# Optimization experiments

Hardware: AMD Instinct MI355X
Metric: run time of the kernel (lower is better)

## Reference

```python
import jax, jax.numpy as jnp
import numpy as np

N = 50000   # nodes per node type
D = 256     # in_dim == out_dim
H = 8       # num heads
DK = D // H # 32
E = 500000  # edges per edge type
LN_EPS = 1e-5


def setup_inputs() -> dict:
    key = jax.random.key(0)
    ks = jax.random.split(key, 16)
    w = lambda k, shape: jax.random.normal(k, shape, dtype=jnp.float32) * 0.05
    xav = np.sqrt(6.0 / (DK + DK))
    return {
        'feats': jax.random.normal(ks[0], (2, N, D), dtype=jnp.float32),
        'Wk': w(ks[1], (2, D, D)), 'bk': jnp.zeros((2, D), jnp.float32),
        'Wq': w(ks[2], (2, D, D)), 'bq': jnp.zeros((2, D), jnp.float32),
        'Wv': w(ks[3], (2, D, D)), 'bv': jnp.zeros((2, D), jnp.float32),
        'Wa': w(ks[4], (2, D, D)), 'ba': jnp.zeros((2, D), jnp.float32),
        'ln_w': jnp.ones((2, D), jnp.float32), 'ln_b': jnp.zeros((2, D), jnp.float32),
        'skip': jnp.ones((2,), jnp.float32),
        'mu': jnp.ones((2, H), jnp.float32),
        'w_att': jax.random.uniform(ks[5], (2, H, DK, DK), jnp.float32, -xav, xav),
        'w_msg': jax.random.uniform(ks[6], (2, H, DK, DK), jnp.float32, -xav, xav),
        'src': jax.random.randint(ks[7], (2, E), 0, N, dtype=jnp.int32),
        'dst': jax.random.randint(ks[8], (2, E), 0, N, dtype=jnp.int32),
    }


def _edge_softmax(scores, seg, n):
    # scores: (E, H); softmax over edges sharing the same destination node
    m = jax.ops.segment_max(scores, seg, num_segments=n)          # (N, H)
    e = jnp.exp(scores - m[seg])
    s = jax.ops.segment_sum(e, seg, num_segments=n)               # (N, H)
    return e / s[seg]


def _forward(feats, Wk, bk, Wq, bq, Wv, bv, Wa, ba, ln_w, ln_b, skip,
             mu, w_att, w_msg, src, dst):
    # canonical etypes: 0 = author->paper, 1 = paper->author
    stypes, dtypes = (0, 1), (1, 0)
    scale = 1.0 / jnp.sqrt(jnp.asarray(DK, feats.dtype))
    h = [None, None]
    for et in range(2):
        st, dt = stypes[et], dtypes[et]
        s_idx, d_idx = src[et], dst[et]
        k = (feats[st] @ Wk[st] + bk[st]).reshape(N, H, DK)
        k = jnp.einsum('nhi,hij->nhj', k, w_att[et])
        v = (feats[st] @ Wv[st] + bv[st]).reshape(N, H, DK)
        v = jnp.einsum('nhi,hij->nhj', v, w_msg[et])
        q = (feats[dt] @ Wq[dt] + bq[dt]).reshape(N, H, DK)
        t = jnp.einsum('ehd,ehd->eh', q[d_idx], k[s_idx])         # (E, H)
        attn = _edge_softmax(t * mu[et] * scale, d_idx, N)        # (E, H)
        msg = v[s_idx] * attn[..., None]                          # (E, H, DK)
        h[dt] = jax.ops.segment_sum(msg, d_idx, num_segments=N).reshape(N, D)
    h = jnp.stack(h)  # (2, N, D); each ntype receives from exactly one etype

    trans = jnp.einsum('tnd,tde->tne', h, Wa) + ba[:, None, :]
    alpha = jax.nn.sigmoid(skip)[:, None, None]
    out = alpha * trans + (1.0 - alpha) * feats
    mean = out.mean(-1, keepdims=True)
    var = out.var(-1, keepdims=True)
    out = (out - mean) * jax.lax.rsqrt(var + LN_EPS)
    return out * ln_w[:, None, :] + ln_b[:, None, :]


def reference(feats, Wk, bk, Wq, bq, Wv, bv, Wa, ba, ln_w, ln_b, skip,
              mu, w_att, w_msg, src, dst):
    return _forward(feats, Wk, bk, Wq, bq, Wv, bv, Wa, ba, ln_w, ln_b, skip,
                    mu, w_att, w_msg, src, dst)
```

## Files before the change

### kernel.cpp

```cpp
#include <hip/hip_runtime.h>
#include <hip/hip_bf16.h>

#define D 256
#define H 8
#define DK 32

typedef unsigned short ushort_t;
typedef unsigned int uint_t;
typedef __attribute__((ext_vector_type(4))) float floatx4;
typedef __attribute__((ext_vector_type(2))) float floatx2;
typedef __attribute__((ext_vector_type(8))) short shortx8;
typedef __attribute__((ext_vector_type(8))) unsigned short ushortx8;

typedef __attribute__((address_space(3))) void lds_void_t;
typedef const __attribute__((address_space(1))) void gbl_void_t;

__device__ __forceinline__ float b2f(ushort_t u) {
    return __uint_as_float(((uint_t)u) << 16);
}
__device__ __forceinline__ floatx2 b2x2(uint_t u) {
    floatx2 r;
    r.x = __uint_as_float(u << 16);
    r.y = __uint_as_float(u & 0xffff0000u);
    return r;
}
__device__ __forceinline__ ushort_t f2b(float f) {
    uint_t u = __float_as_uint(f);
    uint_t r = (u + 0x7FFFu + ((u >> 16) & 1u)) >> 16;
    return (ushort_t)r;
}
__device__ __forceinline__ void async_cp16(const void* g, void* l) {
    __builtin_amdgcn_global_load_lds((gbl_void_t*)g, (lds_void_t*)l, 16, 0, 0);
}

__global__ void cvt_bf16(const float* __restrict__ in, ushort_t* __restrict__ out, size_t n4) {
    size_t i = (size_t)blockIdx.x * blockDim.x + threadIdx.x;
    if (i >= n4) return;
    float4 v = ((const float4*)in)[i];
    ushort4 o;
    o.x = f2b(v.x); o.y = f2b(v.y); o.z = f2b(v.z); o.w = f2b(v.w);
    ((ushort4*)out)[i] = o;
}

__global__ void zero_int(int* __restrict__ p, int n) {
    int i = blockIdx.x * blockDim.x + threadIdx.x;
    if (i < n) p[i] = 0;
}

__global__ void fold_weights(const float* __restrict__ Wk, const float* __restrict__ bk,
                             const float* __restrict__ Wv, const float* __restrict__ bv,
                             const float* __restrict__ w_att, const float* __restrict__ w_msg,
                             float* __restrict__ Wkc, float* __restrict__ bkc,
                             float* __restrict__ Wvc, float* __restrict__ bvc) {
    int r = blockIdx.x, et = blockIdx.y, which = blockIdx.z;
    int tid = threadIdx.x;
    const float* Wsrc = (which ? Wv : Wk) + (size_t)et * D * D + (size_t)r * D;
    const float* wt   = (which ? w_msg : w_att) + (size_t)et * H * DK * DK;
    float* Wdst = (which ? Wvc : Wkc) + (size_t)et * D * D;
    __shared__ float wrow[D];
    wrow[tid] = Wsrc[tid];
    __syncthreads();
    int h = tid >> 5, j = tid & 31;
    const float* wth = wt + h * DK * DK;
    float acc = 0.f;
#pragma unroll 8
    for (int i = 0; i < DK; i++) acc += wrow[h * 32 + i] * wth[i * 32 + j];
    Wdst[(size_t)r * D + tid] = acc;
    if (r == 0) {
        const float* bsrc = (which ? bv : bk) + et * D;
        float* bdst = (which ? bvc : bkc) + et * D;
        float bacc = 0.f;
#pragma unroll 8
        for (int i = 0; i < DK; i++) bacc += bsrc[h * 32 + i] * wth[i * 32 + j];
        bdst[tid] = bacc;
    }
}

__global__ void pack_weights(const float* __restrict__ Wq, const float* __restrict__ bq,
                             const float* __restrict__ Wkc, const float* __restrict__ bkc,
                             const float* __restrict__ Wvc, const float* __restrict__ bvc,
                             const float* __restrict__ Wa,
                             ushort_t* __restrict__ WT_all, ushort_t* __restrict__ WaT,
                             float* __restrict__ bias_all) {
    int idx = blockIdx.x * blockDim.x + threadIdx.x;
    const int NW = 2 * 768 * 256;
    if (idx < NW) {
        int t = idx / (768 * 256);
        int rem = idx - t * 768 * 256;
        int n = rem >> 8, k = rem & 255;
        int sec = n >> 8, nn = n & 255;
        const float* W = (sec == 0) ? Wq : (sec == 1) ? Wkc : Wvc;
        WT_all[idx] = f2b(W[(size_t)t * D * D + (size_t)k * D + nn]);
    } else if (idx < NW + 2 * 256 * 256) {
        int r = idx - NW;
        int t = r / (256 * 256);
        int rem = r - t * 256 * 256;
        int n = rem >> 8, k = rem & 255;
        WaT[r] = f2b(Wa[(size_t)t * D * D + (size_t)k * D + n]);
    }
    if (idx < 2 * 768) {
        int t = idx / 768, n = idx % 768;
        int sec = n >> 8, nn = n & 255;
        const float* b = (sec == 0) ? bq : (sec == 1) ? bkc : bvc;
        bias_all[idx] = b[t * D + nn];
    }
}

#define TM 128
#define TN 128
#define TKK 64
__launch_bounds__(256)
__global__ void gemm_mfma(const ushort_t* __restrict__ A0, int lda, size_t aStr,
                          const ushort_t* __restrict__ BT0, size_t bStr,
                          const float* __restrict__ bias0, int biasStr,
                          ushort_t* __restrict__ C0, int ldc, size_t cStr, int M) {
    __shared__ ushort_t As[TM * TKK];
    __shared__ ushort_t Bs[TN * TKK];
    int tid = threadIdx.x;
    int w = tid >> 6, lane = tid & 63;
    int t = blockIdx.z;
    const ushort_t* A  = A0 + (size_t)t * aStr;
    const ushort_t* BT = BT0 + (size_t)t * bStr;
    const float* bias  = bias0 + (size_t)t * biasStr;
    ushort_t* C        = C0 + (size_t)t * cStr;

    int nwg  = gridDim.x * gridDim.y;
    int orig = blockIdx.y * gridDim.x + blockIdx.x;
    int q = nwg >> 3, r = nwg & 7;
    int xcd = orig & 7, loc = orig >> 3;
    int wgid = (xcd < r ? xcd * (q + 1) : r * (q + 1) + (xcd - r) * q) + loc;
    int ncol = gridDim.y;
    int rowt = wgid / ncol;
    int colt = wgid - rowt * ncol;
    int bm = rowt * TM;
    int bn = colt * TN;

    int wm = (w & 1) * 64, wn = (w >> 1) * 64;

    floatx4 acc[4][4] = {};

    int sr8    = lane >> 3;
    int swzcol = 8 * ((lane & 7) ^ sr8);

    int fr = lane & 15, fq = lane >> 4;
    int fswz = (fr & 7) * 8;

    for (int kc = 0; kc < 256; kc += TKK) {
#pragma unroll
        for (int j = 0; j < 4; j++) {
            int rr = w * 32 + j * 8;
            int gr = bm + rr + sr8; if (gr >= M) gr = M - 1;
            async_cp16(A + (size_t)gr * lda + kc + swzcol, As + rr * TKK);
            int gn = bn + rr + sr8;
            async_cp16(BT + (size_t)gn * 256 + kc + swzcol, Bs + rr * TKK);
        }
        __builtin_amdgcn_s_waitcnt(0x0F70);
        __syncthreads();

#pragma unroll
        for (int kk = 0; kk < 2; kk++) {
            shortx8 af[4], bf[4];
            int rcol = (kk * 32) ^ fswz;
#pragma unroll
            for (int i = 0; i < 4; i++)
                af[i] = *(const shortx8*)(As + (wm + i * 16 + fr) * TKK + ((kk * 32 + fq * 8) ^ fswz));
#pragma unroll
            for (int j = 0; j < 4; j++)
                bf[j] = *(const shortx8*)(Bs + (wn + j * 16 + fr) * TKK + ((kk * 32 + fq * 8) ^ fswz));
#pragma unroll
            for (int i = 0; i < 4; i++)
#pragma unroll
                for (int j = 0; j < 4; j++)
                    acc[i][j] = __builtin_amdgcn_mfma_f32_16x16x32_bf16(af[i], bf[j], acc[i][j], 0, 0, 0);
            (void)rcol;
        }
        __syncthreads();
    }

#pragma unroll
    for (int i = 0; i < 4; i++) {
#pragma unroll
        for (int j = 0; j < 4; j++) {
            int col = bn + wn + j * 16 + fr;
            float bv = bias[col];
#pragma unroll
            for (int rr = 0; rr < 4; rr++) {
                int row = bm + wm + i * 16 + fq * 4 + rr;
                if (row < M) C[(size_t)row * ldc + col] = f2b(acc[i][j][rr] + bv);
            }
        }
    }
}

__global__ void count_deg(const int* __restrict__ dst, int* __restrict__ deg,
                          int N, int E) {
    int i = blockIdx.x * blockDim.x + threadIdx.x;
    if (i >= 2 * E) return;
    int et = i / E, e = i - et * E;
    int d = dst[(size_t)et * E + e];
    atomicAdd(&deg[(1 - et) * N + d], 1);
}

__launch_bounds__(256)
__global__ void scan_blocks(int* __restrict__ deg, int* __restrict__ bsum, int n) {
    __shared__ int wsum[4];
    int tid = threadIdx.x, lane = tid & 63, w = tid >> 6;
    int i = blockIdx.x * 256 + tid;
    int v = (i < n) ? deg[i] : 0;
    int x = v;
#pragma unroll
    for (int off = 1; off < 64; off <<= 1) {
        int y = __shfl_up(x, off);
        if (lane >= off) x += y;
    }
    if (lane == 63) wsum[w] = x;
    __syncthreads();
    int add = 0;
    if (w > 0) add += wsum[0];
    if (w > 1) add += wsum[1];
    if (w > 2) add += wsum[2];
    int incl = x + add;
    if (i < n) deg[i] = incl - v;
    if (tid == 255) bsum[blockIdx.x] = incl;
}

__launch_bounds__(512)
__global__ void scan_tops(int* __restrict__ bsum, int* __restrict__ row_ptr,
                          int nb, int n) {
    __shared__ int wsum[8];
    int tid = threadIdx.x, lane = tid & 63, w = tid >> 6;
    int v = (tid < nb) ? bsum[tid] : 0;
    int x = v;
#pragma unroll
    for (int off = 1; off < 64; off <<= 1) {
        int y = __shfl_up(x, off);
        if (lane >= off) x += y;
    }
    if (lane == 63) wsum[w] = x;
    __syncthreads();
    int add = 0;
    for (int j = 0; j < w; j++) add += wsum[j];
    int incl = x + add;
    if (tid < nb) bsum[tid] = incl - v;
    if (tid == nb - 1) row_ptr[n] = incl;
}

__launch_bounds__(256)
__global__ void scan_apply(const int* __restrict__ excl, const int* __restrict__ bsum,
                           int* __restrict__ row_ptr, int* __restrict__ cursor, int n) {
    int i = blockIdx.x * 256 + threadIdx.x;
    if (i >= n) return;
    int e = excl[i] + bsum[blockIdx.x];
    row_ptr[i] = e;
    cursor[i] = e;
}

__global__ void fill_edges(const int* __restrict__ src, const int* __restrict__ dst,
                           int* __restrict__ cursor, int* __restrict__ ebuf,
                           int N, int E) {
    int i = blockIdx.x * blockDim.x + threadIdx.x;
    if (i >= 2 * E) return;
    int et = i / E, e = i - et * E;
    int d = dst[(size_t)et * E + e];
    int s = src[(size_t)et * E + e];
    int pos = atomicAdd(&cursor[(1 - et) * N + d], 1);
    ebuf[pos] = s;
}

__launch_bounds__(256)
__global__ void node_aggregate(ushort_t* __restrict__ QKV, const float* __restrict__ mu,
                               const int* __restrict__ row_ptr, const int* __restrict__ ebuf,
                               int N) {
    int wid = (blockIdx.x * blockDim.x + threadIdx.x) >> 6;
    int lane = threadIdx.x & 63;
    if (wid >= 2 * N) return;
    int dt = (wid >= N) ? 1 : 0;
    int et = 1 - dt;
    int l = lane & 31;
    int half = lane >> 5;
    int h = l >> 2;

    uint4 qu = ((const uint4*)(QKV + (size_t)wid * 768))[l];
    floatx2 q01 = b2x2(qu.x), q23 = b2x2(qu.y), q45 = b2x2(qu.z), q67 = b2x2(qu.w);
    float sc = mu[et * H + h] * 0.17677669529663687f;
    int beg = row_ptr[wid], end = row_ptr[wid + 1];
    const ushort_t* KVb = QKV + (size_t)et * N * 768 + l * 8;

    floatx2 a01 = {0.f, 0.f}, a23 = {0.f, 0.f}, a45 = {0.f, 0.f}, a67 = {0.f, 0.f};
    float ssum = 0.f;

#define AGG_COMPUTE(kk, vv)                                              \
    {                                                                    \
        floatx2 pv = q01 * b2x2(kk.x);                                   \
        pv += q23 * b2x2(kk.y);                                          \
        pv += q45 * b2x2(kk.z);                                          \
        pv += q67 * b2x2(kk.w);                                          \
        float pp = pv.x + pv.y;                                          \
        pp += __shfl_xor(pp, 1);                                         \
        pp += __shfl_xor(pp, 2);                                         \
        float ex = __expf(pp * sc);                                      \
        ssum += ex;                                                      \
        floatx2 e2 = {ex, ex};                                           \
        a01 += e2 * b2x2(vv.x);                                          \
        a23 += e2 * b2x2(vv.y);                                          \
        a45 += e2 * b2x2(vv.z);                                          \
        a67 += e2 * b2x2(vv.w);                                          \
    }

    int p = beg + half;
    uint4 kA = {}, vA = {}, kB = {}, vB = {};
    int sC = 0, sD = 0;
    if (p < end) {
        int sA = ebuf[p];
        const ushort_t* r0 = KVb + (size_t)sA * 768;
        kA = *(const uint4*)(r0 + 256);
        vA = *(const uint4*)(r0 + 512);
        sC = (p + 4 < end) ? ebuf[p + 4] : sA;
    }
    if (p + 2 < end) {
        int sB = ebuf[p + 2];
        const ushort_t* r1 = KVb + (size_t)sB * 768;
        kB = *(const uint4*)(r1 + 256);
        vB = *(const uint4*)(r1 + 512);
        sD = (p + 6 < end) ? ebuf[p + 6] : sB;
    }
    while (p < end) {
        uint4 nk = kA, nv = vA;
        int sE = sC;
        if (p + 4 < end) {
            const ushort_t* rr = KVb + (size_t)sC * 768;
            nk = *(const uint4*)(rr + 256);
            nv = *(const uint4*)(rr + 512);
            if (p + 8 < end) sE = ebuf[p + 8];
        }
        AGG_COMPUTE(kA, vA);
        kA = nk; vA = nv; sC = sE;
        p += 2;
        if (p >= end) break;
        nk = kB; nv = vB; sE = sD;
        if (p + 4 < end) {
            const ushort_t* rr = KVb + (size_t)sD * 768;
            nk = *(const uint4*)(rr + 256);
            nv = *(const uint4*)(rr + 512);
            if (p + 8 < end) sE = ebuf[p + 8];
        }
        AGG_COMPUTE(kB, vB);
        kB = nk; vB = nv; sD = sE;
        p += 2;
    }
#undef AGG_COMPUTE

    ssum += __shfl_xor(ssum, 32);
    a01.x += __shfl_xor(a01.x, 32); a01.y += __shfl_xor(a01.y, 32);
    a23.x += __shfl_xor(a23.x, 32); a23.y += __shfl_xor(a23.y, 32);
    a45.x += __shfl_xor(a45.x, 32); a45.y += __shfl_xor(a45.y, 32);
    a67.x += __shfl_xor(a67.x, 32); a67.y += __shfl_xor(a67.y, 32);
    float r = (ssum > 0.f) ? 1.0f / ssum : 0.0f;
    if (half == 0) {
        ushortx8 hv;
        hv[0] = f2b(a01.x * r); hv[1] = f2b(a01.y * r);
        hv[2] = f2b(a23.x * r); hv[3] = f2b(a23.y * r);
        hv[4] = f2b(a45.x * r); hv[5] = f2b(a45.y * r);
        hv[6] = f2b(a67.x * r); hv[7] = f2b(a67.y * r);
        ((ushortx8*)(QKV + (size_t)wid * 768))[l] = hv;
    }
}

__launch_bounds__(256)
__global__ void skip_ln(const ushort_t* __restrict__ trans, const float* __restrict__ feats,
                        const float* __restrict__ lnw, const float* __restrict__ lnb,
                        const float* __restrict__ skip, float* __restrict__ out, int N) {
    int wid = (blockIdx.x * blockDim.x + threadIdx.x) >> 6;
    int lane = threadIdx.x & 63;
    if (wid >= 2 * N) return;
    int t = (wid >= N) ? 1 : 0;
    float alpha = 1.0f / (1.0f + __expf(-skip[t]));
    float beta = 1.0f - alpha;
    size_t base = (size_t)wid * D;
    ushort4 tu = ((const ushort4*)(trans + base))[lane];
    float4 fu = ((const float4*)(feats + base))[lane];
    float x0 = alpha * b2f(tu.x) + beta * fu.x;
    float x1 = alpha * b2f(tu.y) + beta * fu.y;
    float x2 = alpha * b2f(tu.z) + beta * fu.z;
    float x3 = alpha * b2f(tu.w) + beta * fu.w;
    float s  = x0 + x1 + x2 + x3;
    float sq = x0 * x0 + x1 * x1 + x2 * x2 + x3 * x3;
#pragma unroll
    for (int off = 1; off < 64; off <<= 1) {
        s  += __shfl_xor(s,  off);
        sq += __shfl_xor(sq, off);
    }
    float mean = s * (1.0f / 256.0f);
    float var  = sq * (1.0f / 256.0f) - mean * mean;
    float r = rsqrtf(var + 1e-5f);
    float4 w4 = ((const float4*)(lnw + t * D))[lane];
    float4 b4 = ((const float4*)(lnb + t * D))[lane];
    float4 o;
    o.x = (x0 - mean) * r * w4.x + b4.x;
    o.y = (x1 - mean) * r * w4.y + b4.y;
    o.z = (x2 - mean) * r * w4.z + b4.z;
    o.w = (x3 - mean) * r * w4.w + b4.w;
    ((float4*)(out + base))[lane] = o;
}

extern "C" void kernel_launch(void* const* d_in, const int* in_sizes, int n_in,
                              void* d_out, int out_size, void* d_ws, size_t ws_size,
                              hipStream_t stream) {
    const float* feats = (const float*)d_in[0];
    const float* Wk    = (const float*)d_in[1];
    const float* bk    = (const float*)d_in[2];
    const float* Wq    = (const float*)d_in[3];
    const float* bq    = (const float*)d_in[4];
    const float* Wv    = (const float*)d_in[5];
    const float* bv    = (const float*)d_in[6];
    const float* Wa    = (const float*)d_in[7];
    const float* ba    = (const float*)d_in[8];
    const float* ln_w  = (const float*)d_in[9];
    const float* ln_b  = (const float*)d_in[10];
    const float* skip  = (const float*)d_in[11];
    const float* mu    = (const float*)d_in[12];
    const float* w_att = (const float*)d_in[13];
    const float* w_msg = (const float*)d_in[14];
    const int*   src   = (const int*)d_in[15];
    const int*   dst   = (const int*)d_in[16];
    float* out = (float*)d_out;

    const int N = in_sizes[0] / (2 * D);
    const int E = in_sizes[15] / 2;
    const int NN = 2 * N;
    const size_t ND2 = 2 * (size_t)N * D;

    float* ws = (float*)d_ws;
    size_t off = 0;
    float* Wkc  = ws + off; off += 2 * (size_t)D * D;
    float* Wvc  = ws + off; off += 2 * (size_t)D * D;
    float* bkc  = ws + off; off += 2 * D;
    float* bvc  = ws + off; off += 2 * D;
    float* bias_all = ws + off; off += 2 * 768;
    ushort_t* WT_all = (ushort_t*)(ws + off); off += 2 * 768 * 256 / 2;
    ushort_t* WaT    = (ushort_t*)(ws + off); off += 2 * 256 * 256 / 2;
    ushort_t* featsb = (ushort_t*)(ws + off); off += ND2 / 2;
    ushort_t* QKV    = (ushort_t*)(ws + off); off += 2 * (size_t)N * 768 / 2;
    int* deg     = (int*)(ws + off); off += NN;
    int* row_ptr = (int*)(ws + off); off += NN + 1;
    int* cursor  = (int*)(ws + off); off += NN + 1;
    int* ebuf    = (int*)(ws + off); off += 2 * (size_t)E;
    int* bsum    = (int*)(ws + off); off += 512;

    const int nb = (NN + 255) / 256;

    zero_int<<<(NN + 255) / 256, 256, 0, stream>>>(deg, NN);
    count_deg<<<(2 * E + 255) / 256, 256, 0, stream>>>(dst, deg, N, E);
    scan_blocks<<<nb, 256, 0, stream>>>(deg, bsum, NN);
    scan_tops<<<1, 512, 0, stream>>>(bsum, row_ptr, nb, NN);
    scan_apply<<<nb, 256, 0, stream>>>(deg, bsum, row_ptr, cursor, NN);
    fill_edges<<<(2 * E + 255) / 256, 256, 0, stream>>>(src, dst, cursor, ebuf, N, E);

    fold_weights<<<dim3(D, 2, 2), 256, 0, stream>>>(Wk, bk, Wv, bv, w_att, w_msg,
                                                    Wkc, bkc, Wvc, bvc);
    pack_weights<<<(2 * 768 * 256 + 2 * 256 * 256 + 255) / 256, 256, 0, stream>>>(
        Wq, bq, Wkc, bkc, Wvc, bvc, Wa, WT_all, WaT, bias_all);

    cvt_bf16<<<(unsigned)((ND2 / 4 + 255) / 256), 256, 0, stream>>>(feats, featsb, ND2 / 4);

    dim3 qkv_grid((N + TM - 1) / TM, 768 / TN, 2);
    gemm_mfma<<<qkv_grid, 256, 0, stream>>>(featsb, D, (size_t)N * D,
                                            WT_all, (size_t)768 * 256,
                                            bias_all, 768,
                                            QKV, 768, (size_t)N * 768, N);

    node_aggregate<<<(NN * 64 + 255) / 256, 256, 0, stream>>>(QKV, mu, row_ptr, ebuf, N);

    ushort_t* transb = featsb;
    dim3 tr_grid((N + TM - 1) / TM, 256 / TN, 2);
    gemm_mfma<<<tr_grid, 256, 0, stream>>>(QKV, 768, (size_t)N * 768,
                                           WaT, (size_t)256 * 256,
                                           ba, 256,
                                           transb, D, (size_t)N * D, N);

    skip_ln<<<(NN * 64 + 255) / 256, 256, 0, stream>>>(transb, feats, ln_w, ln_b, skip, out, N);
}
```

Baseline: 622.0 us.

## Double-buffer GEMM LDS tiles and read bf16 feats in skip-layernorm

The GEMM now uses two LDS buffers with a K-tile of 32, so async copies for the next stage are issued before the MFMAs run on the current one, and the XOR swizzle is dropped. The trans output is written into a spare column slice of the QKV buffer, which leaves the bf16 feats buffer intact. skip_ln then reads bf16 feats instead of fp32 feats, halving that read. Dropping the swizzle may bring back LDS bank conflicts, and reading bf16 feats for the residual lowers its precision.

```diff
diff --git a/kernel.cpp b/kernel.cpp
--- a/kernel.cpp
+++ b/kernel.cpp
@@ -108,14 +108,15 @@
 
 #define TM 128
 #define TN 128
-#define TKK 64
+#define TKK 32
 __launch_bounds__(256)
 __global__ void gemm_mfma(const ushort_t* __restrict__ A0, int lda, size_t aStr,
                           const ushort_t* __restrict__ BT0, size_t bStr,
                           const float* __restrict__ bias0, int biasStr,
-                          ushort_t* __restrict__ C0, int ldc, size_t cStr, int M) {
-    __shared__ ushort_t As[TM * TKK];
-    __shared__ ushort_t Bs[TN * TKK];
+                          ushort_t* __restrict__ C0, int ldc, size_t cStr,
+                          int cShift, int M) {
+    __shared__ ushort_t As[2][TM * TKK];
+    __shared__ ushort_t Bs[2][TN * TKK];
     int tid = threadIdx.x;
     int w = tid >> 6, lane = tid & 63;
     int t = blockIdx.z;
@@ -139,43 +140,49 @@
 
     floatx4 acc[4][4] = {};
 
-    int sr8    = lane >> 3;
-    int swzcol = 8 * ((lane & 7) ^ sr8);
-
+    int srow = lane >> 2;
+    int scol = (lane & 3) * 8;
     int fr = lane & 15, fq = lane >> 4;
-    int fswz = (fr & 7) * 8;
-
-    for (int kc = 0; kc < 256; kc += TKK) {
-#pragma unroll
-        for (int j = 0; j < 4; j++) {
-            int rr = w * 32 + j * 8;
-            int gr = bm + rr + sr8; if (gr >= M) gr = M - 1;
-            async_cp16(A + (size_t)gr * lda + kc + swzcol, As + rr * TKK);
-            int gn = bn + rr + sr8;
-            async_cp16(BT + (size_t)gn * 256 + kc + swzcol, Bs + rr * TKK);
-        }
-        __builtin_amdgcn_s_waitcnt(0x0F70);
-        __syncthreads();
-
-#pragma unroll
-        for (int kk = 0; kk < 2; kk++) {
-            shortx8 af[4], bf[4];
-            int rcol = (kk * 32) ^ fswz;
-#pragma unroll
-            for (int i = 0; i < 4; i++)
-                af[i] = *(const shortx8*)(As + (wm + i * 16 + fr) * TKK + ((kk * 32 + fq * 8) ^ fswz));
-#pragma unroll
-            for (int j = 0; j < 4; j++)
-                bf[j] = *(const shortx8*)(Bs + (wn + j * 16 + fr) * TKK + ((kk * 32 + fq * 8) ^ fswz));
-#pragma unroll
-            for (int i = 0; i < 4; i++)
-#pragma unroll
-                for (int j = 0; j < 4; j++)
-                    acc[i][j] = __builtin_amdgcn_mfma_f32_16x16x32_bf16(af[i], bf[j], acc[i][j], 0, 0, 0);
-            (void)rcol;
+
+#define GEMM_STAGE(b, kc)                                                     \
+    {                                                                         \
+        _Pragma("unroll")                                                     \
+        for (int j = 0; j < 2; j++) {                                         \
+            int rr = w * 32 + j * 16;                                         \
+            int gr = bm + rr + srow; if (gr >= M) gr = M - 1;                 \
+            async_cp16(A + (size_t)gr * lda + (kc) + scol, As[b] + rr * TKK); \
+            int gn = bn + rr + srow;                                          \
+            async_cp16(BT + (size_t)gn * 256 + (kc) + scol, Bs[b] + rr * TKK);\
+        }                                                                     \
+    }
+
+    GEMM_STAGE(0, 0);
+#pragma unroll
+    for (int s = 0; s < 8; s++) {
+        int cur = s & 1;
+        if (s < 7) {
+            GEMM_STAGE(cur ^ 1, (s + 1) * TKK);
+            __builtin_amdgcn_s_waitcnt(0x0F74);
+        } else {
+            __builtin_amdgcn_s_waitcnt(0x0F70);
         }
         __syncthreads();
-    }
+
+        shortx8 af[4], bf[4];
+#pragma unroll
+        for (int i = 0; i < 4; i++)
+            af[i] = *(const shortx8*)(As[cur] + (wm + i * 16 + fr) * TKK + fq * 8);
+#pragma unroll
+        for (int j = 0; j < 4; j++)
+            bf[j] = *(const shortx8*)(Bs[cur] + (wn + j * 16 + fr) * TKK + fq * 8);
+#pragma unroll
+        for (int i = 0; i < 4; i++)
+#pragma unroll
+            for (int j = 0; j < 4; j++)
+                acc[i][j] = __builtin_amdgcn_mfma_f32_16x16x32_bf16(af[i], bf[j], acc[i][j], 0, 0, 0);
+        __syncthreads();
+    }
+#undef GEMM_STAGE
 
 #pragma unroll
     for (int i = 0; i < 4; i++) {
@@ -186,7 +193,7 @@
 #pragma unroll
             for (int rr = 0; rr < 4; rr++) {
                 int row = bm + wm + i * 16 + fq * 4 + rr;
-                if (row < M) C[(size_t)row * ldc + col] = f2b(acc[i][j][rr] + bv);
+                if (row < M) C[(size_t)row * ldc + cShift + col] = f2b(acc[i][j][rr] + bv);
             }
         }
     }
@@ -367,7 +374,7 @@
 }
 
 __launch_bounds__(256)
-__global__ void skip_ln(const ushort_t* __restrict__ trans, const float* __restrict__ feats,
+__global__ void skip_ln(const ushort_t* __restrict__ trans, const ushort_t* __restrict__ featsb,
                         const float* __restrict__ lnw, const float* __restrict__ lnb,
                         const float* __restrict__ skip, float* __restrict__ out, int N) {
     int wid = (blockIdx.x * blockDim.x + threadIdx.x) >> 6;
@@ -376,13 +383,12 @@
     int t = (wid >= N) ? 1 : 0;
     float alpha = 1.0f / (1.0f + __expf(-skip[t]));
     float beta = 1.0f - alpha;
-    size_t base = (size_t)wid * D;
-    ushort4 tu = ((const ushort4*)(trans + base))[lane];
-    float4 fu = ((const float4*)(feats + base))[lane];
-    float x0 = alpha * b2f(tu.x) + beta * fu.x;
-    float x1 = alpha * b2f(tu.y) + beta * fu.y;
-    float x2 = alpha * b2f(tu.z) + beta * fu.z;
-    float x3 = alpha * b2f(tu.w) + beta * fu.w;
+    ushort4 tu = ((const ushort4*)(trans + (size_t)wid * 768))[lane];
+    ushort4 fu = ((const ushort4*)(featsb + (size_t)wid * D))[lane];
+    float x0 = alpha * b2f(tu.x) + beta * b2f(fu.x);
+    float x1 = alpha * b2f(tu.y) + beta * b2f(fu.y);
+    float x2 = alpha * b2f(tu.z) + beta * b2f(fu.z);
+    float x3 = alpha * b2f(tu.w) + beta * b2f(fu.w);
     float s  = x0 + x1 + x2 + x3;
     float sq = x0 * x0 + x1 * x1 + x2 * x2 + x3 * x3;
 #pragma unroll
@@ -400,7 +406,7 @@
     o.y = (x1 - mean) * r * w4.y + b4.y;
     o.z = (x2 - mean) * r * w4.z + b4.z;
     o.w = (x3 - mean) * r * w4.w + b4.w;
-    ((float4*)(out + base))[lane] = o;
+    ((float4*)(out + (size_t)wid * D))[lane] = o;
 }
 
 extern "C" void kernel_launch(void* const* d_in, const int* in_sizes, int n_in,
@@ -467,16 +473,16 @@
     gemm_mfma<<<qkv_grid, 256, 0, stream>>>(featsb, D, (size_t)N * D,
                                             WT_all, (size_t)768 * 256,
                                             bias_all, 768,
-                                            QKV, 768, (size_t)N * 768, N);
+                                            QKV, 768, (size_t)N * 768, 0, N);
 
     node_aggregate<<<(NN * 64 + 255) / 256, 256, 0, stream>>>(QKV, mu, row_ptr, ebuf, N);
 
-    ushort_t* transb = featsb;
     dim3 tr_grid((N + TM - 1) / TM, 256 / TN, 2);
     gemm_mfma<<<tr_grid, 256, 0, stream>>>(QKV, 768, (size_t)N * 768,
                                            WaT, (size_t)256 * 256,
                                            ba, 256,
-                                           transb, D, (size_t)N * D, N);
-
-    skip_ln<<<(NN * 64 + 255) / 256, 256, 0, stream>>>(transb, feats, ln_w, ln_b, skip, out, N);
-}
+                                           QKV, 768, (size_t)N * 768, 256, N);
+
+    skip_ln<<<(NN * 64 + 255) / 256, 256, 0, stream>>>(QKV + 256, featsb,
+                                                       ln_w, ln_b, skip, out, N);
+}
```

Result: faster. 603.5 us (-3.0%).
